# Kernel optimization log

Measured on AMD Instinct MI355X. Metric: run time of the kernel, lower is better.

## Reference

```python
import jax, jax.numpy as jnp
import numpy as np

H = 1.0  # binarization scale (default in module)

def round_through(x):
    # straight-through estimator: forward = round(x), backward = identity
    return x + jax.lax.stop_gradient(jnp.round(x) - x)

def binary_tanh_unit(x):
    hs = jnp.clip((x + 1.0) / 2.0, 0.0, 1.0)  # hard sigmoid
    return 2.0 * round_through(hs) - 1.0

def setup_inputs() -> dict:
    key = jax.random.key(0)
    kx, kw, kb = jax.random.split(key, 3)
    N, d_in, d_out = 16384, 1024, 1024
    x = jax.random.normal(kx, (N, d_in), dtype=jnp.float32)
    # kernel initialized uniform in [-H, H] per the module
    W = jax.random.uniform(kw, (d_in, d_out), dtype=jnp.float32, minval=-H, maxval=H)
    b = jax.random.normal(kb, (d_out,), dtype=jnp.float32) * 0.01
    return {"x": x, "W": W, "b": b}

def reference(x, W, b):
    # binarize weights to +/-H, then dense matmul + bias
    Wb = H * binary_tanh_unit(W / H)  # values in {-H, +H}
    out = jnp.matmul(x, Wb) + b       # [N, d_out]
    return out
```

## Files before the change

### kernel.cpp

```cpp
#include <hip/hip_runtime.h>
#include <stdint.h>

typedef __bf16 bf16_t;
typedef __bf16 bf16x8 __attribute__((ext_vector_type(8)));
typedef float f32x4 __attribute__((ext_vector_type(4)));
typedef unsigned short ushort8 __attribute__((ext_vector_type(8)));

#define M_DIM 16384
#define N_DIM 1024
#define K_DIM 1024
#define BM 256
#define BN 256
#define BK 64
#define NT (K_DIM / BK)
#define AELEM (BM * BK)

__global__ void cvt_x_bf16(const float* __restrict__ x,
                           unsigned short* __restrict__ xb, int n8) {
    int i = blockIdx.x * blockDim.x + threadIdx.x;
    int stride = gridDim.x * blockDim.x;
    for (; i < n8; i += stride) {
        const float4* p = (const float4*)(x + (size_t)i * 8);
        float4 v0 = p[0], v1 = p[1];
        float vv[8] = {v0.x, v0.y, v0.z, v0.w, v1.x, v1.y, v1.z, v1.w};
        ushort8 o;
#pragma unroll
        for (int j = 0; j < 8; ++j) {
            uint32_t u = __builtin_bit_cast(uint32_t, vv[j]);
            u = u + 0x7FFFu + ((u >> 16) & 1u);
            o[j] = (unsigned short)(u >> 16);
        }
        *(ushort8*)(xb + (size_t)i * 8) = o;
    }
}

__global__ void bin_transpose_w(const float* __restrict__ W,
                                unsigned short* __restrict__ WbT) {
    __shared__ unsigned short t[64][68];
    int tj = blockIdx.x;
    int ti = blockIdx.y;
    int tid = threadIdx.x;
    int c4 = (tid & 15) * 4;
    int r0 = tid >> 4;
#pragma unroll
    for (int p = 0; p < 4; ++p) {
        int r = r0 + p * 16;
        float4 v = *(const float4*)(W + (size_t)(ti * 64 + r) * N_DIM + tj * 64 + c4);
        t[r][c4 + 0] = ((v.x + 1.0f) * 0.5f > 0.5f) ? 0x3F80 : 0xBF80;
        t[r][c4 + 1] = ((v.y + 1.0f) * 0.5f > 0.5f) ? 0x3F80 : 0xBF80;
        t[r][c4 + 2] = ((v.z + 1.0f) * 0.5f > 0.5f) ? 0x3F80 : 0xBF80;
        t[r][c4 + 3] = ((v.w + 1.0f) * 0.5f > 0.5f) ? 0x3F80 : 0xBF80;
    }
    __syncthreads();
#pragma unroll
    for (int p = 0; p < 4; ++p) {
        int rn = r0 + p * 16;
        ushort4 o;
        o.x = t[c4 + 0][rn];
        o.y = t[c4 + 1][rn];
        o.z = t[c4 + 2][rn];
        o.w = t[c4 + 3][rn];
        *(ushort4*)(WbT + (size_t)(tj * 64 + rn) * K_DIM + ti * 64 + c4) = o;
    }
}

__device__ __forceinline__ void gload16(const bf16_t* g, const bf16_t* l) {
    __builtin_amdgcn_global_load_lds(
        (const __attribute__((address_space(1))) void*)(g),
        (__attribute__((address_space(3))) void*)(l),
        16, 0, 0);
}

#define PHASE_BODY(P, S0, S1)                                                   \
    {                                                                           \
        bf16x8 afr[2][2];                                                       \
        _Pragma("unroll") for (int i = 0; i < 2; ++i)                           \
            _Pragma("unroll") for (int k = 0; k < 2; ++k)                       \
                afr[i][k] = *(const bf16x8*)(Ab + (wr * 128 + ((P)*2 + i) * 16 + lr) * BK \
                                             + (((k * 4 + lk) ^ l7) * 8));      \
        S0; S1;                                                                 \
        __builtin_amdgcn_s_barrier();                                           \
        asm volatile("s_waitcnt lgkmcnt(0)" ::: "memory");                      \
        __builtin_amdgcn_sched_barrier(0);                                      \
        __builtin_amdgcn_s_setprio(1);                                          \
        _Pragma("unroll") for (int i = 0; i < 2; ++i)                           \
            _Pragma("unroll") for (int n = 0; n < 4; ++n)                       \
                _Pragma("unroll") for (int k = 0; k < 2; ++k)                   \
                    acc[(P)*2 + i][n] = __builtin_amdgcn_mfma_f32_16x16x32_bf16(\
                        afr[i][k], bfr[n][k], acc[(P)*2 + i][n], 0, 0, 0);      \
        __builtin_amdgcn_s_setprio(0);                                          \
    }

__global__ __launch_bounds__(512, 2) void bgemm(const bf16_t* __restrict__ A,
                                                const bf16_t* __restrict__ Bt,
                                                const float* __restrict__ bias,
                                                float* __restrict__ C) {
    __shared__ __align__(16) bf16_t lds[5 * AELEM];

    const int nwg = (M_DIM / BM) * (N_DIM / BN);
    int bid = blockIdx.x;
    int swz = (bid & 7) * (nwg >> 3) + (bid >> 3);
    int tile_n = swz & 3;
    int tile_m = swz >> 2;
    int bm0 = tile_m * BM;
    int bn0 = tile_n * BN;

    int tid = threadIdx.x;
    int w = tid >> 6, l = tid & 63;
    int wr = w >> 2, wc = w & 3;
    int lr = l & 15, lk = l >> 4, l7 = l & 7;

    int srow = tid >> 3;
    int schunk = (tid & 7) ^ (srow & 7);
    auto stageA1 = [&](int t, int c) {
        gload16(A + (size_t)(bm0 + c * 64 + srow) * K_DIM + t * BK + schunk * 8,
                lds + (t % 3) * AELEM + c * 4096 + tid * 8);
    };
    auto stageB1 = [&](int t, int c) {
        gload16(Bt + (size_t)(bn0 + c * 64 + srow) * K_DIM + t * BK + schunk * 8,
                lds + (3 + (t & 1)) * AELEM + c * 4096 + tid * 8);
    };

    f32x4 acc[8][4];
#pragma unroll
    for (int m = 0; m < 8; ++m)
#pragma unroll
        for (int n = 0; n < 4; ++n)
            acc[m][n] = (f32x4)(0.0f);

#pragma unroll
    for (int c = 0; c < 4; ++c) stageA1(0, c);
#pragma unroll
    for (int c = 0; c < 4; ++c) stageB1(0, c);
#pragma unroll
    for (int c = 0; c < 4; ++c) stageA1(1, c);
    asm volatile("s_waitcnt vmcnt(4)" ::: "memory");
    __builtin_amdgcn_s_barrier();

    for (int t = 0; t < NT; ++t) {
        const bf16_t* Ab = lds + (t % 3) * AELEM;
        const bf16_t* Bb = lds + (3 + (t & 1)) * AELEM;
        bool pfB = (t + 1) < NT;
        bool pfA = (t + 2) < NT;

        bf16x8 bfr[4][2];
#pragma unroll
        for (int n = 0; n < 4; ++n)
#pragma unroll
            for (int k = 0; k < 2; ++k)
                bfr[n][k] = *(const bf16x8*)(Bb + (wc * 64 + n * 16 + lr) * BK
                                             + (((k * 4 + lk) ^ l7) * 8));

        PHASE_BODY(0, if (pfB) stageB1(t + 1, 0), if (pfB) stageB1(t + 1, 1));
        __builtin_amdgcn_s_barrier();
        PHASE_BODY(1, if (pfB) stageB1(t + 1, 2), if (pfB) stageB1(t + 1, 3));
        __builtin_amdgcn_s_barrier();
        PHASE_BODY(2, if (pfA) stageA1(t + 2, 0), if (pfA) stageA1(t + 2, 1));
        __builtin_amdgcn_s_barrier();
        PHASE_BODY(3, if (pfA) stageA1(t + 2, 2), if (pfA) stageA1(t + 2, 3));

        if (t + 1 < NT) {
            if (t + 2 < NT)
                asm volatile("s_waitcnt vmcnt(4)" ::: "memory");
            else
                asm volatile("s_waitcnt vmcnt(0)" ::: "memory");
            __builtin_amdgcn_s_barrier();
        }
    }

#pragma unroll
    for (int n = 0; n < 4; ++n) {
        int col = bn0 + wc * 64 + n * 16 + lr;
        float bv = bias[col];
#pragma unroll
        for (int m = 0; m < 8; ++m) {
            int row0 = bm0 + wr * 128 + m * 16 + lk * 4;
#pragma unroll
            for (int j = 0; j < 4; ++j)
                C[(size_t)(row0 + j) * N_DIM + col] = acc[m][n][j] + bv;
        }
    }
}

__global__ void naive_bin_dense(const float* __restrict__ x,
                                const float* __restrict__ W,
                                const float* __restrict__ b,
                                float* __restrict__ out) {
    int col = blockIdx.x * 256 + threadIdx.x;
    int row = blockIdx.y;
    float acc = 0.0f;
    for (int k = 0; k < K_DIM; ++k) {
        float s = ((W[(size_t)k * N_DIM + col] + 1.0f) * 0.5f > 0.5f) ? 1.0f : -1.0f;
        acc += x[(size_t)row * K_DIM + k] * s;
    }
    out[(size_t)row * N_DIM + col] = acc + b[col];
}

extern "C" void kernel_launch(void* const* d_in, const int* in_sizes, int n_in,
                              void* d_out, int out_size, void* d_ws, size_t ws_size,
                              hipStream_t stream) {
    const float* x = (const float*)d_in[0];
    const float* W = (const float*)d_in[1];
    const float* b = (const float*)d_in[2];
    float* out = (float*)d_out;

    size_t xb_bytes = (size_t)M_DIM * K_DIM * sizeof(unsigned short);
    size_t wb_bytes = (size_t)K_DIM * N_DIM * sizeof(unsigned short);

    if (ws_size >= xb_bytes + wb_bytes) {
        unsigned short* xb = (unsigned short*)d_ws;
        unsigned short* wbt = (unsigned short*)((char*)d_ws + xb_bytes);
        hipLaunchKernelGGL(bin_transpose_w, dim3(N_DIM / 64, K_DIM / 64), dim3(256),
                           0, stream, W, wbt);
        hipLaunchKernelGGL(cvt_x_bf16, dim3(2048), dim3(256), 0, stream,
                           x, xb, (M_DIM * K_DIM) / 8);
        hipLaunchKernelGGL(bgemm, dim3((M_DIM / BM) * (N_DIM / BN)), dim3(512), 0, stream,
                           (const bf16_t*)xb, (const bf16_t*)wbt, b, out);
    } else {
        hipLaunchKernelGGL(naive_bin_dense, dim3(N_DIM / 256, M_DIM), dim3(256),
                           0, stream, x, W, b, out);
    }
}
```

Baseline: 61.77 us.

## Replace phased barrier-interleaved main loop with bulk prefetch and plain MFMA loop

Removes the four-phase schedule that interleaved global-to-LDS prefetch with MFMA groups under intra-iteration barriers, setprio and sched_barrier. All next-tile B and A loads are now issued at the top of the iteration, followed by a simple unrolled loop that loads A fragments per row block and runs the MFMAs. This cuts barrier and scheduling-fence overhead and lets the compiler interleave freely. In exchange it loses explicit overlap control and priority hints, and may bunch memory traffic.

```diff
diff --git a/kernel.cpp b/kernel.cpp
--- a/kernel.cpp
+++ b/kernel.cpp
@@ -70,26 +70,6 @@
         (__attribute__((address_space(3))) void*)(l),
         16, 0, 0);
 }
-
-#define PHASE_BODY(P, S0, S1)                                                   \
-    {                                                                           \
-        bf16x8 afr[2][2];                                                       \
-        _Pragma("unroll") for (int i = 0; i < 2; ++i)                           \
-            _Pragma("unroll") for (int k = 0; k < 2; ++k)                       \
-                afr[i][k] = *(const bf16x8*)(Ab + (wr * 128 + ((P)*2 + i) * 16 + lr) * BK \
-                                             + (((k * 4 + lk) ^ l7) * 8));      \
-        S0; S1;                                                                 \
-        __builtin_amdgcn_s_barrier();                                           \
-        asm volatile("s_waitcnt lgkmcnt(0)" ::: "memory");                      \
-        __builtin_amdgcn_sched_barrier(0);                                      \
-        __builtin_amdgcn_s_setprio(1);                                          \
-        _Pragma("unroll") for (int i = 0; i < 2; ++i)                           \
-            _Pragma("unroll") for (int n = 0; n < 4; ++n)                       \
-                _Pragma("unroll") for (int k = 0; k < 2; ++k)                   \
-                    acc[(P)*2 + i][n] = __builtin_amdgcn_mfma_f32_16x16x32_bf16(\
-                        afr[i][k], bfr[n][k], acc[(P)*2 + i][n], 0, 0, 0);      \
-        __builtin_amdgcn_s_setprio(0);                                          \
-    }
 
 __global__ __launch_bounds__(512, 2) void bgemm(const bf16_t* __restrict__ A,
                                                 const bf16_t* __restrict__ Bt,
@@ -140,8 +120,15 @@
     for (int t = 0; t < NT; ++t) {
         const bf16_t* Ab = lds + (t % 3) * AELEM;
         const bf16_t* Bb = lds + (3 + (t & 1)) * AELEM;
-        bool pfB = (t + 1) < NT;
-        bool pfA = (t + 2) < NT;
+
+        if (t + 1 < NT) {
+#pragma unroll
+            for (int c = 0; c < 4; ++c) stageB1(t + 1, c);
+        }
+        if (t + 2 < NT) {
+#pragma unroll
+            for (int c = 0; c < 4; ++c) stageA1(t + 2, c);
+        }
 
         bf16x8 bfr[4][2];
 #pragma unroll
@@ -150,14 +137,20 @@
             for (int k = 0; k < 2; ++k)
                 bfr[n][k] = *(const bf16x8*)(Bb + (wc * 64 + n * 16 + lr) * BK
                                              + (((k * 4 + lk) ^ l7) * 8));
-
-        PHASE_BODY(0, if (pfB) stageB1(t + 1, 0), if (pfB) stageB1(t + 1, 1));
-        __builtin_amdgcn_s_barrier();
-        PHASE_BODY(1, if (pfB) stageB1(t + 1, 2), if (pfB) stageB1(t + 1, 3));
-        __builtin_amdgcn_s_barrier();
-        PHASE_BODY(2, if (pfA) stageA1(t + 2, 0), if (pfA) stageA1(t + 2, 1));
-        __builtin_amdgcn_s_barrier();
-        PHASE_BODY(3, if (pfA) stageA1(t + 2, 2), if (pfA) stageA1(t + 2, 3));
+#pragma unroll
+        for (int m = 0; m < 8; ++m) {
+            bf16x8 afr[2];
+#pragma unroll
+            for (int k = 0; k < 2; ++k)
+                afr[k] = *(const bf16x8*)(Ab + (wr * 128 + m * 16 + lr) * BK
+                                          + (((k * 4 + lk) ^ l7) * 8));
+#pragma unroll
+            for (int n = 0; n < 4; ++n)
+#pragma unroll
+                for (int k = 0; k < 2; ++k)
+                    acc[m][n] = __builtin_amdgcn_mfma_f32_16x16x32_bf16(
+                        afr[k], bfr[n][k], acc[m][n], 0, 0, 0);
+        }
 
         if (t + 1 < NT) {
             if (t + 2 < NT)
```

New measurement: 61.91 us. No clear change (+0.2%).

## Restructure GEMM pipeline to double-buffered A/B LDS with unrolled two-tile loop

Applied to the files above, without the earlier changes.

Replaces the triple-buffered A / double-buffered B LDS scheme with a unified double buffer of A and B per K-tile. The main loop is unrolled by two tiles, giving eight phases per iteration, and prefetch issue is reordered so A for tile t+1 and B for tile t+2 load during compute. B fragment reads are folded into phase 0 with a partial lgkmcnt wait. The goal is a smoother overlap of global-to-LDS loads with MFMA and simpler buffer indexing, at the risk of different LDS usage and tighter wait and barrier ordering.

```diff
diff --git a/kernel.cpp b/kernel.cpp
--- a/kernel.cpp
+++ b/kernel.cpp
@@ -13,7 +13,8 @@
 #define BN 256
 #define BK 64
 #define NT (K_DIM / BK)
-#define AELEM (BM * BK)
+#define BUF_B 65536
+#define B_OFF 32768
 
 __global__ void cvt_x_bf16(const float* __restrict__ x,
                            unsigned short* __restrict__ xb, int n8) {
@@ -64,38 +65,18 @@
     }
 }
 
-__device__ __forceinline__ void gload16(const bf16_t* g, const bf16_t* l) {
+__device__ __forceinline__ void gload16(const void* g, const void* l) {
     __builtin_amdgcn_global_load_lds(
         (const __attribute__((address_space(1))) void*)(g),
         (__attribute__((address_space(3))) void*)(l),
         16, 0, 0);
 }
 
-#define PHASE_BODY(P, S0, S1)                                                   \
-    {                                                                           \
-        bf16x8 afr[2][2];                                                       \
-        _Pragma("unroll") for (int i = 0; i < 2; ++i)                           \
-            _Pragma("unroll") for (int k = 0; k < 2; ++k)                       \
-                afr[i][k] = *(const bf16x8*)(Ab + (wr * 128 + ((P)*2 + i) * 16 + lr) * BK \
-                                             + (((k * 4 + lk) ^ l7) * 8));      \
-        S0; S1;                                                                 \
-        __builtin_amdgcn_s_barrier();                                           \
-        asm volatile("s_waitcnt lgkmcnt(0)" ::: "memory");                      \
-        __builtin_amdgcn_sched_barrier(0);                                      \
-        __builtin_amdgcn_s_setprio(1);                                          \
-        _Pragma("unroll") for (int i = 0; i < 2; ++i)                           \
-            _Pragma("unroll") for (int n = 0; n < 4; ++n)                       \
-                _Pragma("unroll") for (int k = 0; k < 2; ++k)                   \
-                    acc[(P)*2 + i][n] = __builtin_amdgcn_mfma_f32_16x16x32_bf16(\
-                        afr[i][k], bfr[n][k], acc[(P)*2 + i][n], 0, 0, 0);      \
-        __builtin_amdgcn_s_setprio(0);                                          \
-    }
-
 __global__ __launch_bounds__(512, 2) void bgemm(const bf16_t* __restrict__ A,
                                                 const bf16_t* __restrict__ Bt,
                                                 const float* __restrict__ bias,
                                                 float* __restrict__ C) {
-    __shared__ __align__(16) bf16_t lds[5 * AELEM];
+    __shared__ __align__(16) char lds[2 * BUF_B];
 
     const int nwg = (M_DIM / BM) * (N_DIM / BN);
     int bid = blockIdx.x;
@@ -112,13 +93,19 @@
 
     int srow = tid >> 3;
     int schunk = (tid & 7) ^ (srow & 7);
-    auto stageA1 = [&](int t, int c) {
-        gload16(A + (size_t)(bm0 + c * 64 + srow) * K_DIM + t * BK + schunk * 8,
-                lds + (t % 3) * AELEM + c * 4096 + tid * 8);
+    auto stageAh = [&](int t, int h) {
+#pragma unroll
+        for (int c = 0; c < 2; ++c)
+            gload16(A + (size_t)(bm0 + h * 128 + c * 64 + srow) * K_DIM
+                        + t * BK + schunk * 8,
+                    lds + (t & 1) * BUF_B + h * 16384 + c * 8192 + tid * 16);
     };
-    auto stageB1 = [&](int t, int c) {
-        gload16(Bt + (size_t)(bn0 + c * 64 + srow) * K_DIM + t * BK + schunk * 8,
-                lds + (3 + (t & 1)) * AELEM + c * 4096 + tid * 8);
+    auto stageBh = [&](int t, int h) {
+#pragma unroll
+        for (int c = 0; c < 2; ++c)
+            gload16(Bt + (size_t)(bn0 + h * 128 + c * 64 + srow) * K_DIM
+                         + t * BK + schunk * 8,
+                    lds + (t & 1) * BUF_B + B_OFF + h * 16384 + c * 8192 + tid * 16);
     };
 
     f32x4 acc[8][4];
@@ -128,45 +115,62 @@
         for (int n = 0; n < 4; ++n)
             acc[m][n] = (f32x4)(0.0f);
 
-#pragma unroll
-    for (int c = 0; c < 4; ++c) stageA1(0, c);
-#pragma unroll
-    for (int c = 0; c < 4; ++c) stageB1(0, c);
-#pragma unroll
-    for (int c = 0; c < 4; ++c) stageA1(1, c);
+    bf16x8 bfr[4][2];
+
+#define PHASE(TILE, PP, STAGE, WAIT)                                            \
+    {                                                                           \
+        const char* Ar = lds + ((TILE) & 1) * BUF_B + wr * 16384;               \
+        bf16x8 afr[2][2];                                                       \
+        _Pragma("unroll") for (int i = 0; i < 2; ++i)                           \
+            _Pragma("unroll") for (int kk = 0; kk < 2; ++kk)                    \
+                afr[i][kk] = *(const bf16x8*)(Ar + (((PP) * 2 + i) * 16 + lr) * 128 \
+                                              + (((kk * 4 + lk) ^ l7) * 16));   \
+        if ((PP) == 0) {                                                        \
+            const char* Br = lds + ((TILE) & 1) * BUF_B + B_OFF + (wc >> 1) * 16384; \
+            _Pragma("unroll") for (int n = 0; n < 4; ++n)                       \
+                _Pragma("unroll") for (int kk = 0; kk < 2; ++kk)                \
+                    bfr[n][kk] = *(const bf16x8*)(Br + ((wc & 1) * 64 + n * 16 + lr) * 128 \
+                                                  + (((kk * 4 + lk) ^ l7) * 16)); \
+        }                                                                       \
+        STAGE;                                                                  \
+        if ((PP) == 0) asm volatile("s_waitcnt lgkmcnt(8)" ::: "memory");       \
+        __builtin_amdgcn_s_barrier();                                           \
+        asm volatile("s_waitcnt lgkmcnt(0)" ::: "memory");                      \
+        __builtin_amdgcn_sched_barrier(0);                                      \
+        __builtin_amdgcn_s_setprio(1);                                          \
+        _Pragma("unroll") for (int i = 0; i < 2; ++i)                           \
+            _Pragma("unroll") for (int n = 0; n < 4; ++n)                       \
+                _Pragma("unroll") for (int kk = 0; kk < 2; ++kk)                \
+                    acc[(PP) * 2 + i][n] = __builtin_amdgcn_mfma_f32_16x16x32_bf16( \
+                        afr[i][kk], bfr[n][kk], acc[(PP) * 2 + i][n], 0, 0, 0); \
+        __builtin_amdgcn_s_setprio(0);                                          \
+        WAIT;                                                                   \
+        __builtin_amdgcn_s_barrier();                                           \
+    }
+
+    stageAh(0, 0); stageAh(0, 1);
+    stageBh(0, 0); stageBh(0, 1);
+    stageBh(1, 0); stageBh(1, 1);
     asm volatile("s_waitcnt vmcnt(4)" ::: "memory");
     __builtin_amdgcn_s_barrier();
 
-    for (int t = 0; t < NT; ++t) {
-        const bf16_t* Ab = lds + (t % 3) * AELEM;
-        const bf16_t* Bb = lds + (3 + (t & 1)) * AELEM;
-        bool pfB = (t + 1) < NT;
-        bool pfA = (t + 2) < NT;
-
-        bf16x8 bfr[4][2];
-#pragma unroll
-        for (int n = 0; n < 4; ++n)
-#pragma unroll
-            for (int k = 0; k < 2; ++k)
-                bfr[n][k] = *(const bf16x8*)(Bb + (wc * 64 + n * 16 + lr) * BK
-                                             + (((k * 4 + lk) ^ l7) * 8));
-
-        PHASE_BODY(0, if (pfB) stageB1(t + 1, 0), if (pfB) stageB1(t + 1, 1));
-        __builtin_amdgcn_s_barrier();
-        PHASE_BODY(1, if (pfB) stageB1(t + 1, 2), if (pfB) stageB1(t + 1, 3));
-        __builtin_amdgcn_s_barrier();
-        PHASE_BODY(2, if (pfA) stageA1(t + 2, 0), if (pfA) stageA1(t + 2, 1));
-        __builtin_amdgcn_s_barrier();
-        PHASE_BODY(3, if (pfA) stageA1(t + 2, 2), if (pfA) stageA1(t + 2, 3));
-
-        if (t + 1 < NT) {
-            if (t + 2 < NT)
-                asm volatile("s_waitcnt vmcnt(4)" ::: "memory");
-            else
-                asm volatile("s_waitcnt vmcnt(0)" ::: "memory");
-            __builtin_amdgcn_s_barrier();
-        }
-    }
+    for (int it = 0; it < NT / 2; ++it) {
+        int t0 = it * 2, t1 = t0 + 1;
+        bool pf0 = (t0 + 2) < NT, pf1 = (t1 + 2) < NT;
+
+        PHASE(t0, 0, stageAh(t1, 0), );
+        PHASE(t0, 1, stageAh(t1, 1), );
+        PHASE(t0, 2, if (pf0) stageBh(t0 + 2, 0), );
+        PHASE(t0, 3, if (pf0) stageBh(t0 + 2, 1),
+              if (pf0) asm volatile("s_waitcnt vmcnt(4)" ::: "memory");
+              else     asm volatile("s_waitcnt vmcnt(0)" ::: "memory"););
+        PHASE(t1, 0, if (pf0) stageAh(t0 + 2, 0), );
+        PHASE(t1, 1, if (pf0) stageAh(t0 + 2, 1), );
+        PHASE(t1, 2, if (pf1) stageBh(t1 + 2, 0), );
+        PHASE(t1, 3, if (pf1) stageBh(t1 + 2, 1),
+              if (pf1) asm volatile("s_waitcnt vmcnt(4)" ::: "memory"););
+    }
+#undef PHASE
 
 #pragma unroll
     for (int n = 0; n < 4; ++n) {
```

Result: faster. 60.36 us (-2.3%).
